# Performance work log

Hardware: AMD Instinct MI355X
Metric: run time of the kernel (lower is better)

Reference implementation:

```python
import jax, jax.numpy as jnp
import numpy as np
from jax import lax

EPS = 1e-5

def setup_inputs() -> dict:
    key = jax.random.key(0)
    k1, k2 = jax.random.split(key)
    x = jax.random.normal(k1, (8, 256, 64, 64), dtype=jnp.float32)
    W = jax.random.normal(k2, (128, 256, 5, 5), dtype=jnp.float32) * 0.02
    gamma = jnp.ones((128,), dtype=jnp.float32)
    beta = jnp.zeros((128,), dtype=jnp.float32)
    return {"x": x, "W": W, "gamma": gamma, "beta": beta}

def reference(x, W, gamma, beta):
    B, C, H, Wd = x.shape
    # bilinear x2 upsample, half-pixel centers (== torch align_corners=False)
    up = jax.image.resize(x, (B, C, 2 * H, 2 * Wd), method="bilinear")
    # conv2d, stride 1, padding 2, no bias (norm == 'BN')
    out = lax.conv_general_dilated(
        up, W, window_strides=(1, 1), padding=[(2, 2), (2, 2)],
        dimension_numbers=("NCHW", "OIHW", "NCHW"))
    # BatchNorm2d (batch statistics, training-style refresh)
    mean = jnp.mean(out, axis=(0, 2, 3))
    var = jnp.var(out, axis=(0, 2, 3))
    inv = gamma / jnp.sqrt(var + EPS)
    out = (out - mean[None, :, None, None]) * inv[None, :, None, None] + beta[None, :, None, None]
    # activation: torch.relu
    return jax.nn.relu(out)
```

## Files before the change

### kernel.cpp

```cpp
#include <hip/hip_runtime.h>
#include <hip/hip_bf16.h>
#include <stdint.h>

typedef short s8v __attribute__((ext_vector_type(8)));
typedef float f4v __attribute__((ext_vector_type(4)));

__device__ __forceinline__ void async_copy16(const void* gsrc, void* lds_dst) {
  __builtin_amdgcn_global_load_lds(
      (const __attribute__((address_space(1))) uint32_t*)(uintptr_t)gsrc,
      (__attribute__((address_space(3))) uint32_t*)(uint32_t)(uintptr_t)lds_dst,
      16, 0, 0);
}

#define WAITVM(N) asm volatile("s_waitcnt vmcnt(" #N ")" ::: "memory")
__device__ __forceinline__ void block_barrier() {
  asm volatile("" ::: "memory");
  __builtin_amdgcn_s_barrier();
  asm volatile("" ::: "memory");
}

__global__ __launch_bounds__(256) void wpack_kernel(const float* __restrict__ W,
                                                    __hip_bfloat16* __restrict__ Wr,
                                                    float* __restrict__ gstats) {
  __shared__ __hip_bfloat16 t[256 * 26];
  const int co = blockIdx.x;
  const int tid = threadIdx.x;
  if (co == 0) gstats[tid] = 0.f;
  const float* src = W + co * 6400;
  for (int i = tid; i < 6400; i += 256) {
    int ci = i / 25;
    int pos = i - ci * 25;
    t[ci * 26 + pos] = __float2bfloat16(src[i]);
  }
  __syncthreads();
  for (int pos = 0; pos < 25; ++pos)
    Wr[pos * 32768 + co * 256 + tid] = t[tid * 26 + pos];
}

__global__ __launch_bounds__(256, 2) void upsample_kernel(const float* __restrict__ x,
                                                          __hip_bfloat16* __restrict__ up) {
  __shared__ __hip_bfloat16 lx[10 * 48 * 66];
  const int tid = threadIdx.x;
  const int bx = blockIdx.x;
  const int owb = bx & 1;
  const int ohb = (bx >> 1) & 7;
  const int cb = (bx >> 4) & 3;
  const int b = bx >> 6;
  const int oh0 = ohb * 16, ow0 = owb * 64, c0 = cb * 64;
  const int ih0 = (oh0 >> 1) - 1;
  const int iw_lo = (ow0 >> 1) - 1;
  const int aligned = (iw_lo < 0 ? 0 : iw_lo) & ~15;

  for (int i = tid; i < 64 * 10 * 12; i += 256) {
    int c = i / 120;
    int rem = i - c * 120;
    int r = rem / 12;
    int w4 = (rem - r * 12) * 4;
    int gr = ih0 + r;
    gr = gr < 0 ? 0 : (gr > 63 ? 63 : gr);
    const float4 v = *(const float4*)&x[(((b * 256 + c0 + c) * 64) + gr) * 64 + aligned + w4];
    int base = (r * 48 + w4) * 66 + c;
    lx[base]       = __float2bfloat16(v.x);
    lx[base + 66]  = __float2bfloat16(v.y);
    lx[base + 132] = __float2bfloat16(v.z);
    lx[base + 198] = __float2bfloat16(v.w);
  }
  __syncthreads();

  const int c2 = (tid & 31) * 2;
  const int owq = tid >> 5;
  uint32_t* upu = (uint32_t*)up;
  for (int it = 0; it < 128; ++it) {
    int oh_l = it >> 3;
    int ow_l = (it & 7) * 8 + owq;
    int oh = oh0 + oh_l, ow = ow0 + ow_l;
    int ihA = (oh >> 1) - ((oh & 1) ^ 1);
    float wh = (oh & 1) ? 0.75f : 0.25f;
    int iwA = (ow >> 1) - ((ow & 1) ^ 1);
    float wwt = (ow & 1) ? 0.75f : 0.25f;
    int r0 = ihA - ih0;
    int w0 = (iwA < 0 ? 0 : iwA) - aligned;
    int w1t = iwA + 1; w1t = w1t > 63 ? 63 : w1t;
    int w1 = w1t - aligned;
    uint32_t t00 = *(const uint32_t*)&lx[(r0 * 48 + w0) * 66 + c2];
    uint32_t t01 = *(const uint32_t*)&lx[(r0 * 48 + w1) * 66 + c2];
    uint32_t t10 = *(const uint32_t*)&lx[((r0 + 1) * 48 + w0) * 66 + c2];
    uint32_t t11 = *(const uint32_t*)&lx[((r0 + 1) * 48 + w1) * 66 + c2];
    float wlo = wh * wwt, wlo1 = wh * (1.f - wwt);
    float whi = (1.f - wh) * wwt, whi1 = (1.f - wh) * (1.f - wwt);
    float vlo = wlo * __uint_as_float(t00 << 16) + wlo1 * __uint_as_float(t01 << 16) +
                whi * __uint_as_float(t10 << 16) + whi1 * __uint_as_float(t11 << 16);
    float vhi = wlo * __uint_as_float(t00 & 0xffff0000u) + wlo1 * __uint_as_float(t01 & 0xffff0000u) +
                whi * __uint_as_float(t10 & 0xffff0000u) + whi1 * __uint_as_float(t11 & 0xffff0000u);
    __hip_bfloat16 h0 = __float2bfloat16(vlo);
    __hip_bfloat16 h1 = __float2bfloat16(vhi);
    uint32_t pk = (uint32_t)(*(unsigned short*)&h0) | ((uint32_t)(*(unsigned short*)&h1) << 16);
    upu[((((size_t)(b * 128 + oh) * 128) + ow) * 256 + c0 + c2) >> 1] = pk;
  }
}

#define ASLOT 8448
__global__ __launch_bounds__(512, 2) void conv_kernel(const __hip_bfloat16* __restrict__ up,
                                                      const __hip_bfloat16* __restrict__ Wr,
                                                      float* __restrict__ out,
                                                      float* __restrict__ gstats) {
  __shared__ __align__(16) unsigned short lA[5 * ASLOT];
  __shared__ __align__(16) unsigned short lB[3][128 * 64];
  __shared__ float lsum[128], lssq[128];

  const int tid = threadIdx.x;
  const int lane = tid & 63;
  const int wave = tid >> 6;
  const int wm = wave >> 1;
  const int wn = wave & 1;
  const int lane15 = lane & 15;
  const int quad = lane >> 4;
  const int wb = wave << 6;

  const int bid = blockIdx.x;
  const int orig = ((bid & 7) << 5) | (bid >> 3);
  const int b = orig >> 5;
  const int oh0 = (orig & 31) << 2;

  const f4v zero4 = {0.f, 0.f, 0.f, 0.f};
  if (tid < 128) { lsum[tid] = 0.f; lssq[tid] = 0.f; }
  if (tid < 160) {
    int s = tid >> 5, j = tid & 31;
    int rsel = j >> 3;
    int r = (rsel < 2) ? rsel : (128 + rsel);
    *(f4v*)&lA[s * ASLOT + (r * 8 + (j & 7)) * 8] = zero4;
  }

  auto stageA = [&](int slot, const __hip_bfloat16* uprow) {
#pragma unroll
    for (int t = 0; t < 2; ++t) {
      int pl = t * 512 + wb + lane;
      int riw = pl >> 3, pc = pl & 7;
      int r = riw + 2;
      int cq = pc ^ (r & 7);
      async_copy16(uprow + riw * 256 + cq * 8, (void*)&lA[slot * ASLOT + (16 + t * 512 + wb) * 8]);
    }
  };
  auto stageB = [&](const __hip_bfloat16* wsrc, int bsel) {
#pragma unroll
    for (int t = 0; t < 2; ++t) {
      int pl = t * 512 + wb + lane;
      int n = pl >> 3, pc = pl & 7;
      int cq = pc ^ (n & 7);
      async_copy16(wsrc + n * 256 + cq * 8, (void*)&lB[bsel][(t * 512 + wb) * 8]);
    }
  };

  f4v acc[8][4];
#pragma unroll
  for (int i = 0; i < 8; ++i)
#pragma unroll
    for (int j = 0; j < 4; ++j) acc[i][j] = zero4;

  for (int rr = 0; rr < 4; ++rr) {
    int ih = oh0 + rr - 2;
    if ((unsigned)ih < 128u)
      stageA(ih % 5, up + (size_t)(b * 128 + ih) * 32768);
  }
  stageB(Wr, 0);
  __syncthreads();

  int bcur = 0;
  for (int cb = 0; cb < 4; ++cb) {
    const int c0 = cb << 6;
    for (int kh = 0; kh < 5; ++kh) {
      const int ih = oh0 + wm + kh - 2;
      const bool rowok = (unsigned)ih < 128u;
      const int abase = rowok ? (ih % 5) * ASLOT : 0;
      for (int kw = 0; kw < 5; ++kw) {
        const int pos = kh * 5 + kw;
        const int bnext = (bcur == 2) ? 0 : bcur + 1;
        if (cb != 0 && kh == 0 && kw == 0) {
          for (int rr = 0; rr < 4; ++rr) {
            int ihn = oh0 + rr - 2;
            if ((unsigned)ihn < 128u)
              stageA(ihn % 5, up + (size_t)(b * 128 + ihn) * 32768 + c0);
          }
        }
        if (pos < 24)      stageB(Wr + (size_t)(pos + 1) * 32768 + c0, bnext);
        else if (cb < 3)   stageB(Wr + (c0 + 64), bnext);
        const bool extraA = (kw == 2) && (kh < 4) && (oh0 + kh + 2 < 128);
        if (extraA)
          stageA((oh0 + kh + 2) % 5, up + (size_t)(b * 128 + oh0 + kh + 2) * 32768 + c0);
        if (pos == 24 && cb == 3) { WAITVM(0); }
        else if (extraA)          { WAITVM(4); }
        else                      { WAITVM(2); }
        block_barrier();
        if (rowok) {
          __builtin_amdgcn_s_setprio(1);
#pragma unroll
          for (int ks = 0; ks < 2; ++ks) {
            const int cq = ks * 4 + quad;
            s8v a[8], bb[4];
#pragma unroll
            for (int mt = 0; mt < 8; ++mt) {
              int r = mt * 16 + lane15 + kw;
              a[mt] = *(const s8v*)&lA[abase + (r * 8 + (cq ^ (r & 7))) * 8];
            }
#pragma unroll
            for (int nt = 0; nt < 4; ++nt) {
              int n = (wn << 6) + nt * 16 + lane15;
              bb[nt] = *(const s8v*)&lB[bcur][(n * 8 + (cq ^ (n & 7))) * 8];
            }
#pragma unroll
            for (int mt = 0; mt < 8; ++mt)
#pragma unroll
              for (int nt = 0; nt < 4; ++nt)
                acc[mt][nt] = __builtin_amdgcn_mfma_f32_16x16x32_bf16(a[mt], bb[nt], acc[mt][nt], 0, 0, 0);
          }
          __builtin_amdgcn_s_setprio(0);
        }
        if (pos == 24 && cb < 3) block_barrier();
        bcur = bnext;
      }
    }
  }

  const int oh = oh0 + wm;
#pragma unroll
  for (int nt = 0; nt < 4; ++nt) {
    const int n = (wn << 6) + nt * 16 + lane15;
    float* oc = out + ((size_t)(b * 128 + n) * 128 + oh) * 128;
    float s = 0.f, ss = 0.f;
#pragma unroll
    for (int mt = 0; mt < 8; ++mt) {
      f4v v = acc[mt][nt];
      *(f4v*)&oc[mt * 16 + (quad << 2)] = v;
      s += v.x + v.y + v.z + v.w;
      ss += v.x * v.x + v.y * v.y + v.z * v.z + v.w * v.w;
    }
    s += __shfl_xor(s, 16, 64); ss += __shfl_xor(ss, 16, 64);
    s += __shfl_xor(s, 32, 64); ss += __shfl_xor(ss, 32, 64);
    if (quad == 0) { atomicAdd(&lsum[n], s); atomicAdd(&lssq[n], ss); }
  }
  __syncthreads();
  if (tid < 128) {
    atomicAdd(&gstats[tid], lsum[tid]);
    atomicAdd(&gstats[128 + tid], lssq[tid]);
  }
}

__global__ __launch_bounds__(256) void norm_kernel(float* __restrict__ out,
                                                   const float* __restrict__ gstats,
                                                   const float* __restrict__ gamma,
                                                   const float* __restrict__ beta) {
  for (int i = blockIdx.x * 256 + threadIdx.x; i < 4194304; i += 2048 * 256) {
    f4v v = ((f4v*)out)[i];
    int c = (i >> 12) & 127;
    float mean = gstats[c] * (1.f / 131072.f);
    float var = gstats[128 + c] * (1.f / 131072.f) - mean * mean;
    float sc = gamma[c] * rsqrtf(var + 1e-5f);
    float bi = beta[c] - mean * sc;
    v.x = fmaxf(fmaf(v.x, sc, bi), 0.f);
    v.y = fmaxf(fmaf(v.y, sc, bi), 0.f);
    v.z = fmaxf(fmaf(v.z, sc, bi), 0.f);
    v.w = fmaxf(fmaf(v.w, sc, bi), 0.f);
    ((f4v*)out)[i] = v;
  }
}

extern "C" void kernel_launch(void* const* d_in, const int* in_sizes, int n_in,
                              void* d_out, int out_size, void* d_ws, size_t ws_size,
                              hipStream_t stream) {
  (void)in_sizes; (void)n_in; (void)out_size; (void)ws_size;
  const float* x = (const float*)d_in[0];
  const float* W = (const float*)d_in[1];
  const float* gamma = (const float*)d_in[2];
  const float* beta = (const float*)d_in[3];
  float* out = (float*)d_out;
  char* ws = (char*)d_ws;
  __hip_bfloat16* up = (__hip_bfloat16*)ws;
  __hip_bfloat16* Wr = (__hip_bfloat16*)(ws + 67108864);
  float* gstats = (float*)(ws + 67108864 + 1638400);

  wpack_kernel<<<128, 256, 0, stream>>>(W, Wr, gstats);
  upsample_kernel<<<512, 256, 0, stream>>>(x, up);
  conv_kernel<<<256, 512, 0, stream>>>(up, Wr, out, gstats);
  norm_kernel<<<2048, 256, 0, stream>>>(out, gstats, gamma, beta);
}
```

Measured before the change: 297.2 us.

## Fuse BatchNorm+ReLU into conv via grid barrier, halve upsample tile height

The conv kernel now keeps its accumulators in registers, accumulates the channel statistics, waits at a software grid-wide barrier (an atomic counter with spin-wait), then applies the normalisation and ReLU and writes the output once. This removes the separate norm pass, which re-read and re-wrote the 64MB fp32 output. The stats and barrier counter are zeroed with a memset. The upsample kernel also switches to 8-row tiles with twice as many blocks and a smaller LDS footprint. The barrier relies on all 256 conv blocks being co-resident and risks deadlock if they are not.

```diff
diff --git a/kernel.cpp b/kernel.cpp
--- a/kernel.cpp
+++ b/kernel.cpp
@@ -19,13 +19,24 @@
   asm volatile("" ::: "memory");
 }
 
+__device__ __forceinline__ void grid_barrier(int* ctr) {
+  __threadfence();
+  __syncthreads();
+  if (threadIdx.x == 0) {
+    atomicAdd(ctr, 1);
+    while (__hip_atomic_load(ctr, __ATOMIC_ACQUIRE, __HIP_MEMORY_SCOPE_AGENT) < 256) {
+      __builtin_amdgcn_s_sleep(8);
+    }
+  }
+  __syncthreads();
+  __threadfence();
+}
+
 __global__ __launch_bounds__(256) void wpack_kernel(const float* __restrict__ W,
-                                                    __hip_bfloat16* __restrict__ Wr,
-                                                    float* __restrict__ gstats) {
+                                                    __hip_bfloat16* __restrict__ Wr) {
   __shared__ __hip_bfloat16 t[256 * 26];
   const int co = blockIdx.x;
   const int tid = threadIdx.x;
-  if (co == 0) gstats[tid] = 0.f;
   const float* src = W + co * 6400;
   for (int i = tid; i < 6400; i += 256) {
     int ci = i / 25;
@@ -37,23 +48,23 @@
     Wr[pos * 32768 + co * 256 + tid] = t[tid * 26 + pos];
 }
 
-__global__ __launch_bounds__(256, 2) void upsample_kernel(const float* __restrict__ x,
-                                                          __hip_bfloat16* __restrict__ up) {
-  __shared__ __hip_bfloat16 lx[10 * 48 * 66];
+__global__ __launch_bounds__(256) void upsample_kernel(const float* __restrict__ x,
+                                                       __hip_bfloat16* __restrict__ up) {
+  __shared__ __hip_bfloat16 lx[6 * 48 * 66];
   const int tid = threadIdx.x;
   const int bx = blockIdx.x;
   const int owb = bx & 1;
-  const int ohb = (bx >> 1) & 7;
-  const int cb = (bx >> 4) & 3;
-  const int b = bx >> 6;
-  const int oh0 = ohb * 16, ow0 = owb * 64, c0 = cb * 64;
+  const int ohb = (bx >> 1) & 15;
+  const int cb = (bx >> 5) & 3;
+  const int b = bx >> 7;
+  const int oh0 = ohb * 8, ow0 = owb * 64, c0 = cb * 64;
   const int ih0 = (oh0 >> 1) - 1;
   const int iw_lo = (ow0 >> 1) - 1;
   const int aligned = (iw_lo < 0 ? 0 : iw_lo) & ~15;
 
-  for (int i = tid; i < 64 * 10 * 12; i += 256) {
-    int c = i / 120;
-    int rem = i - c * 120;
+  for (int i = tid; i < 64 * 6 * 12; i += 256) {
+    int c = i / 72;
+    int rem = i - c * 72;
     int r = rem / 12;
     int w4 = (rem - r * 12) * 4;
     int gr = ih0 + r;
@@ -70,7 +81,7 @@
   const int c2 = (tid & 31) * 2;
   const int owq = tid >> 5;
   uint32_t* upu = (uint32_t*)up;
-  for (int it = 0; it < 128; ++it) {
+  for (int it = 0; it < 64; ++it) {
     int oh_l = it >> 3;
     int ow_l = (it & 7) * 8 + owq;
     int oh = oh0 + oh_l, ow = ow0 + ow_l;
@@ -103,7 +114,10 @@
 __global__ __launch_bounds__(512, 2) void conv_kernel(const __hip_bfloat16* __restrict__ up,
                                                       const __hip_bfloat16* __restrict__ Wr,
                                                       float* __restrict__ out,
-                                                      float* __restrict__ gstats) {
+                                                      float* __restrict__ gstats,
+                                                      const float* __restrict__ gamma,
+                                                      const float* __restrict__ beta,
+                                                      int* __restrict__ bar) {
   __shared__ __align__(16) unsigned short lA[5 * ASLOT];
   __shared__ __align__(16) unsigned short lB[3][128 * 64];
   __shared__ float lsum[128], lssq[128];
@@ -221,16 +235,13 @@
     }
   }
 
-  const int oh = oh0 + wm;
 #pragma unroll
   for (int nt = 0; nt < 4; ++nt) {
     const int n = (wn << 6) + nt * 16 + lane15;
-    float* oc = out + ((size_t)(b * 128 + n) * 128 + oh) * 128;
     float s = 0.f, ss = 0.f;
 #pragma unroll
     for (int mt = 0; mt < 8; ++mt) {
       f4v v = acc[mt][nt];
-      *(f4v*)&oc[mt * 16 + (quad << 2)] = v;
       s += v.x + v.y + v.z + v.w;
       ss += v.x * v.x + v.y * v.y + v.z * v.z + v.w * v.w;
     }
@@ -243,24 +254,27 @@
     atomicAdd(&gstats[tid], lsum[tid]);
     atomicAdd(&gstats[128 + tid], lssq[tid]);
   }
-}
-
-__global__ __launch_bounds__(256) void norm_kernel(float* __restrict__ out,
-                                                   const float* __restrict__ gstats,
-                                                   const float* __restrict__ gamma,
-                                                   const float* __restrict__ beta) {
-  for (int i = blockIdx.x * 256 + threadIdx.x; i < 4194304; i += 2048 * 256) {
-    f4v v = ((f4v*)out)[i];
-    int c = (i >> 12) & 127;
-    float mean = gstats[c] * (1.f / 131072.f);
-    float var = gstats[128 + c] * (1.f / 131072.f) - mean * mean;
-    float sc = gamma[c] * rsqrtf(var + 1e-5f);
-    float bi = beta[c] - mean * sc;
-    v.x = fmaxf(fmaf(v.x, sc, bi), 0.f);
-    v.y = fmaxf(fmaf(v.y, sc, bi), 0.f);
-    v.z = fmaxf(fmaf(v.z, sc, bi), 0.f);
-    v.w = fmaxf(fmaf(v.w, sc, bi), 0.f);
-    ((f4v*)out)[i] = v;
+
+  grid_barrier(bar);
+
+  const int oh = oh0 + wm;
+#pragma unroll
+  for (int nt = 0; nt < 4; ++nt) {
+    const int n = (wn << 6) + nt * 16 + lane15;
+    float mean = gstats[n] * (1.f / 131072.f);
+    float var = gstats[128 + n] * (1.f / 131072.f) - mean * mean;
+    float sc = gamma[n] * rsqrtf(var + 1e-5f);
+    float bi = beta[n] - mean * sc;
+    float* oc = out + ((size_t)(b * 128 + n) * 128 + oh) * 128;
+#pragma unroll
+    for (int mt = 0; mt < 8; ++mt) {
+      f4v v = acc[mt][nt];
+      v.x = fmaxf(fmaf(v.x, sc, bi), 0.f);
+      v.y = fmaxf(fmaf(v.y, sc, bi), 0.f);
+      v.z = fmaxf(fmaf(v.z, sc, bi), 0.f);
+      v.w = fmaxf(fmaf(v.w, sc, bi), 0.f);
+      *(f4v*)&oc[mt * 16 + (quad << 2)] = v;
+    }
   }
 }
 
@@ -277,9 +291,10 @@
   __hip_bfloat16* up = (__hip_bfloat16*)ws;
   __hip_bfloat16* Wr = (__hip_bfloat16*)(ws + 67108864);
   float* gstats = (float*)(ws + 67108864 + 1638400);
-
-  wpack_kernel<<<128, 256, 0, stream>>>(W, Wr, gstats);
-  upsample_kernel<<<512, 256, 0, stream>>>(x, up);
-  conv_kernel<<<256, 512, 0, stream>>>(up, Wr, out, gstats);
-  norm_kernel<<<2048, 256, 0, stream>>>(out, gstats, gamma, beta);
-}
+  int* bar = (int*)(gstats + 256);
+
+  hipMemsetAsync(gstats, 0, 256 * sizeof(float) + sizeof(int), stream);
+  wpack_kernel<<<128, 256, 0, stream>>>(W, Wr);
+  upsample_kernel<<<1024, 256, 0, stream>>>(x, up);
+  conv_kernel<<<256, 512, 0, stream>>>(up, Wr, out, gstats, gamma, beta, bar);
+}
```

Result: slower. 350.5 us (+18.0%).
